# Performance work log

Hardware: AMD Instinct MI355X
Metric: run time of the kernel (lower is better)

The kernel has to match this reference:

```python
import jax, jax.numpy as jnp
import numpy as np

N_AE = 512
N_DE = 256
N = 100000
NUM_SEG = 1024
EPS = 1e-5


def setup_inputs() -> dict:
    key = jax.random.key(0)
    ks = jax.random.split(key, 20)
    d_in1 = 2 * N_AE + N_DE  # 1280
    inp = {
        "x": jax.random.normal(ks[0], (N, 2 * N_AE), dtype=jnp.float32),
        "dist_feat": jax.random.normal(ks[1], (N, N_DE), dtype=jnp.float32),
        "atom_idx": jax.random.randint(ks[2], (N,), 0, 100, dtype=jnp.int32),
        "ele_idx": jax.random.randint(ks[3], (N,), 0, NUM_SEG, dtype=jnp.int32),
        # layer 1 params
        "l1_w": jax.random.normal(ks[4], (d_in1, N_AE), dtype=jnp.float32) * (1.0 / np.sqrt(d_in1)),
        "l1_b": jnp.zeros((N_AE,), dtype=jnp.float32),
        "l1_g": jnp.ones((N_AE,), dtype=jnp.float32),
        "l1_be": jnp.zeros((N_AE,), dtype=jnp.float32),
        # layer 2 params (same input width: 2*n_ae + n_de)
        "l2_w": jax.random.normal(ks[5], (d_in1, N_AE), dtype=jnp.float32) * (1.0 / np.sqrt(d_in1)),
        "l2_b": jnp.zeros((N_AE,), dtype=jnp.float32),
        "l2_g": jnp.ones((N_AE,), dtype=jnp.float32),
        "l2_be": jnp.zeros((N_AE,), dtype=jnp.float32),
        # final fc + bn
        "f_w": jax.random.normal(ks[6], (2 * N_AE, N_AE), dtype=jnp.float32) * (1.0 / np.sqrt(2 * N_AE)),
        "f_b": jnp.zeros((N_AE,), dtype=jnp.float32),
        "f_g": jnp.ones((N_AE,), dtype=jnp.float32),
        "f_be": jnp.zeros((N_AE,), dtype=jnp.float32),
    }
    return inp


def _bn(h, gamma, beta):
    # BatchNorm1d in training mode: batch stats, biased variance
    m = jnp.mean(h, axis=0)
    v = jnp.mean(jnp.square(h - m), axis=0)
    return gamma * (h - m) * jax.lax.rsqrt(v + EPS) + beta


def _dist_layer(x_cat, ele_idx, w, b, gamma, beta):
    h = jax.nn.relu(_bn(x_cat @ w + b, gamma, beta))  # [N, n_ae]
    sums = jax.ops.segment_sum(h, ele_idx, num_segments=NUM_SEG)  # [S, n_ae]
    cnt = jax.ops.segment_sum(jnp.ones((h.shape[0],), h.dtype), ele_idx, num_segments=NUM_SEG)
    mean = sums / jnp.maximum(cnt, 1.0)[:, None]
    return jnp.concatenate([h, mean[ele_idx]], axis=1)  # [N, 2*n_ae]


def reference(x, dist_feat, atom_idx, ele_idx,
              l1_w, l1_b, l1_g, l1_be,
              l2_w, l2_b, l2_g, l2_be,
              f_w, f_b, f_g, f_be):
    h = _dist_layer(jnp.concatenate([x, dist_feat], axis=1), ele_idx, l1_w, l1_b, l1_g, l1_be)
    h = _dist_layer(jnp.concatenate([h, dist_feat], axis=1), ele_idx, l2_w, l2_b, l2_g, l2_be)
    out = jax.nn.relu(_bn(h @ f_w + f_b, f_g, f_be))  # [N, n_ae]
    return out
```

## Files before the change

### kernel.cpp

```cpp
#include <hip/hip_runtime.h>
#include <stdint.h>
#include <stdio.h>

#define NOUT 512
#define NSEG 1024

typedef unsigned short u16;
typedef __attribute__((ext_vector_type(4))) float f32x4;
typedef __attribute__((ext_vector_type(8))) short s16x8;
typedef __attribute__((ext_vector_type(4))) unsigned short u16x4;

__device__ __forceinline__ u16 f2b(float f) {
  union { float f; uint32_t u; } v; v.f = f;
  uint32_t r = v.u + 0x7FFFu + ((v.u >> 16) & 1u);
  return (u16)(r >> 16);
}
__device__ __forceinline__ float b2f(u16 b) {
  union { uint32_t u; float f; } v; v.u = ((uint32_t)b) << 16;
  return v.f;
}

typedef __attribute__((address_space(1))) const void GAS;
typedef __attribute__((address_space(3))) void LAS;
__device__ __forceinline__ void llds16(const void* g, void* l) {
  __builtin_amdgcn_global_load_lds((GAS*)g, (LAS*)l, 16, 0, 0);
}

__global__ void k_cast(const float* __restrict__ src, u16* __restrict__ dst, long n4) {
  long i = blockIdx.x * (long)blockDim.x + threadIdx.x;
  long stride = (long)gridDim.x * blockDim.x;
  for (; i < n4; i += stride) {
    float4 v = reinterpret_cast<const float4*>(src)[i];
    u16x4 o;
    o.x = f2b(v.x); o.y = f2b(v.y); o.z = f2b(v.z); o.w = f2b(v.w);
    reinterpret_cast<u16x4*>(dst)[i] = o;
  }
}

__global__ void k_wtcastT(const float* __restrict__ w, u16* __restrict__ out, int K) {
  __shared__ float tile[32][33];
  int k0 = blockIdx.x * 32, c0 = blockIdx.y * 32;
  int t = threadIdx.x;
  int rr = t >> 5, cc = t & 31;
#pragma unroll
  for (int p = 0; p < 4; ++p)
    tile[p * 8 + rr][cc] = w[(long)(k0 + p * 8 + rr) * NOUT + c0 + cc];
  __syncthreads();
#pragma unroll
  for (int p = 0; p < 4; ++p)
    out[(long)(c0 + p * 8 + rr) * K + k0 + cc] = f2b(tile[cc][p * 8 + rr]);
}

__global__ void k_hist(const int* __restrict__ ele, int* __restrict__ cnt, int N) {
  int i = blockIdx.x * blockDim.x + threadIdx.x;
  int stride = gridDim.x * blockDim.x;
  for (; i < N; i += stride) atomicAdd(&cnt[ele[i]], 1);
}

__global__ void k_scan(const int* __restrict__ cnt, int* __restrict__ off) {
  __shared__ int tmp[NSEG];
  int t = threadIdx.x;
  tmp[t] = cnt[t];
  __syncthreads();
  for (int o = 1; o < NSEG; o <<= 1) {
    int add = (t >= o) ? tmp[t - o] : 0;
    __syncthreads();
    tmp[t] += add;
    __syncthreads();
  }
  off[t] = tmp[t] - cnt[t];
}

__global__ void k_scatter(const int* __restrict__ ele, const int* __restrict__ off,
                          int* __restrict__ fill, int* __restrict__ rows, int N) {
  int i = blockIdx.x * blockDim.x + threadIdx.x;
  int stride = gridDim.x * blockDim.x;
  for (; i < N; i += stride) {
    int e = ele[i];
    int p = atomicAdd(&fill[e], 1);
    rows[off[e] + p] = i;
  }
}

__global__ void k_finalize(const float* __restrict__ sum, const float* __restrict__ sumsq,
                           const float* __restrict__ g, const float* __restrict__ be,
                           float* __restrict__ A, float* __restrict__ C, int M) {
  int c = threadIdx.x;
  float m = sum[c] / (float)M;
  float v = sumsq[c] / (float)M - m * m;
  float a = g[c] * rsqrtf(v + 1e-5f);
  A[c] = a;
  C[c] = be[c] - a * m;
}

__global__ void k_bnseg(const u16* __restrict__ hp, u16* __restrict__ h, u16* __restrict__ mean,
                        const float* __restrict__ A, const float* __restrict__ C,
                        const int* __restrict__ off, const int* __restrict__ cnt,
                        const int* __restrict__ rows) {
  int s = blockIdx.x;
  int c0 = 2 * threadIdx.x;
  int n = cnt[s], o = off[s];
  float a0 = A[c0], a1 = A[c0 + 1], cc0 = C[c0], cc1 = C[c0 + 1];
  float s0 = 0.f, s1 = 0.f;
#pragma unroll 2
  for (int j = 0; j < n; ++j) {
    int r = rows[o + j];
    uint32_t v = *reinterpret_cast<const uint32_t*>(&hp[(long)r * NOUT + c0]);
    float h0 = fmaxf(a0 * b2f((u16)(v & 0xffff)) + cc0, 0.f);
    float h1 = fmaxf(a1 * b2f((u16)(v >> 16)) + cc1, 0.f);
    s0 += h0; s1 += h1;
    *reinterpret_cast<uint32_t*>(&h[(long)r * NOUT + c0]) =
        ((uint32_t)f2b(h1) << 16) | (uint32_t)f2b(h0);
  }
  float inv = 1.f / fmaxf((float)n, 1.f);
  *reinterpret_cast<uint32_t*>(&mean[(long)s * NOUT + c0]) =
      ((uint32_t)f2b(s1 * inv) << 16) | (uint32_t)f2b(s0 * inv);
}

__global__ void k_final(const u16* __restrict__ hp, float* __restrict__ out,
                        const float* __restrict__ A, const float* __restrict__ C, long n4) {
  long i = blockIdx.x * (long)blockDim.x + threadIdx.x;
  long stride = (long)gridDim.x * blockDim.x;
  for (; i < n4; i += stride) {
    u16x4 v = reinterpret_cast<const u16x4*>(hp)[i];
    int c0 = (int)((i * 4) & (NOUT - 1));
    float4 a = *reinterpret_cast<const float4*>(&A[c0]);
    float4 c = *reinterpret_cast<const float4*>(&C[c0]);
    float4 o;
    o.x = fmaxf(a.x * b2f(v.x) + c.x, 0.f);
    o.y = fmaxf(a.y * b2f(v.y) + c.y, 0.f);
    o.z = fmaxf(a.z * b2f(v.z) + c.z, 0.f);
    o.w = fmaxf(a.w * b2f(v.w) + c.w, 0.f);
    reinterpret_cast<float4*>(out)[i] = o;
  }
}

__global__ __launch_bounds__(256, 4) void k_gemm(
    const u16* p0, const u16* p1, int e0, int w0, int w1, int g0, int g1,
    const int* __restrict__ ele,
    const u16* __restrict__ wbt, int ldb, int e0b, int bskip,
    const float* __restrict__ tab, int addtab,
    u16* __restrict__ outp, float* __restrict__ outf, int wf32,
    float* __restrict__ csum, float* __restrict__ csq, int dostats,
    int M, int K) {
  __shared__ __align__(16) u16 As[2 * 4096];
  __shared__ __align__(16) u16 Bs[2 * 4096];

  int nwg = gridDim.x;
  int orig = blockIdx.x;
  int q = nwg >> 3, r8 = nwg & 7;
  int xcd = orig & 7, loc = orig >> 3;
  int bid = (xcd < r8 ? xcd * (q + 1) : r8 * (q + 1) + (xcd - r8) * q) + loc;
  int mt = bid >> 2, ct = bid & 3;
  int brow = mt * 128, bcol = ct * 128;

  int tid = (int)threadIdx.x;
  int lane = tid & 63;
  int wid = tid >> 6;
  int wr = wid >> 1, wc = wid & 1;
  int l15 = lane & 15, kg = lane >> 4;

  int srow = tid >> 2;
  int soct = ((tid & 3) ^ ((srow >> 1) & 3)) * 8;

  int gr0 = brow + srow, gr1 = gr0 + 64;
  int gr0c = gr0 < M ? gr0 : M - 1;
  int gr1c = gr1 < M ? gr1 : M - 1;
  int el0 = ele[gr0c], el1 = ele[gr1c];

  const u16* a00 = p0 + (long)(g0 ? el0 : gr0c) * w0 + soct;
  const u16* a01 = p1 + (long)(g1 ? el0 : gr0c) * w1 + soct - e0;
  const u16* a10 = p0 + (long)(g0 ? el1 : gr1c) * w0 + soct;
  const u16* a11 = p1 + (long)(g1 ? el1 : gr1c) * w1 + soct - e0;

  const u16* b0p = wbt + (long)(bcol + srow) * ldb + soct;
  const u16* b1p = wbt + (long)(bcol + srow + 64) * ldb + soct;

  int xoct = (kg ^ ((l15 >> 1) & 3)) * 8;
  int aro = (wr * 64 + l15) * 32 + xoct;
  int bro = (wc * 64 + l15) * 32 + xoct;

  f32x4 acc[4][4];
#pragma unroll
  for (int m = 0; m < 4; ++m)
#pragma unroll
    for (int n = 0; n < 4; ++n)
#pragma unroll
      for (int j = 0; j < 4; ++j) acc[m][n][j] = 0.f;

  int KT = K >> 5;
  int dst = wid * 512;

  auto stage = [&](int tt, int buf) {
    int k0 = tt << 5;
    const u16* sa0 = k0 < e0 ? a00 : a01;
    const u16* sa1 = k0 < e0 ? a10 : a11;
    int bo = k0 + (k0 >= e0b ? bskip : 0);
    int ab = buf * 4096 + dst;
    llds16(sa0 + k0, &As[ab]);
    llds16(sa1 + k0, &As[ab + 2048]);
    llds16(b0p + bo, &Bs[ab]);
    llds16(b1p + bo, &Bs[ab + 2048]);
  };

  stage(0, 0);
  __syncthreads();

  for (int t = 0; t < KT; ++t) {
    int cur = t & 1;
    if (t + 1 < KT) stage(t + 1, cur ^ 1);
    __builtin_amdgcn_sched_barrier(0);
    const u16* Ab = &As[cur * 4096];
    const u16* Bb = &Bs[cur * 4096];
    s16x8 af[4], bf[4];
#pragma unroll
    for (int m = 0; m < 4; ++m)
      af[m] = *reinterpret_cast<const s16x8*>(&Ab[m * 512 + aro]);
#pragma unroll
    for (int n = 0; n < 4; ++n)
      bf[n] = *reinterpret_cast<const s16x8*>(&Bb[n * 512 + bro]);
#pragma unroll
    for (int m = 0; m < 4; ++m)
#pragma unroll
      for (int n = 0; n < 4; ++n)
        acc[m][n] = __builtin_amdgcn_mfma_f32_16x16x32_bf16(af[m], bf[n], acc[m][n], 0, 0, 0);
    __syncthreads();
  }

  float sums[4] = {0.f, 0.f, 0.f, 0.f}, sqs[4] = {0.f, 0.f, 0.f, 0.f};
#pragma unroll
  for (int m = 0; m < 4; ++m) {
    int row0 = brow + wr * 64 + m * 16 + kg * 4;
#pragma unroll
    for (int j = 0; j < 4; ++j) {
      int r = row0 + j;
      if (r < M) {
        long rb = (long)r * NOUT;
        long tb = addtab ? (long)ele[r] * NOUT : 0;
#pragma unroll
        for (int n = 0; n < 4; ++n) {
          int col = bcol + wc * 64 + n * 16 + l15;
          float v = acc[m][n][j];
          if (addtab) v += tab[tb + col];
          if (wf32) outf[rb + col] = v;
          else outp[rb + col] = f2b(v);
          sums[n] += v;
          sqs[n] += v * v;
        }
      }
    }
  }
  if (dostats) {
#pragma unroll
    for (int n = 0; n < 4; ++n) {
      sums[n] += __shfl_xor(sums[n], 16);
      sums[n] += __shfl_xor(sums[n], 32);
      sqs[n] += __shfl_xor(sqs[n], 16);
      sqs[n] += __shfl_xor(sqs[n], 32);
    }
    if (kg == 0) {
#pragma unroll
      for (int n = 0; n < 4; ++n) {
        int col = bcol + wc * 64 + n * 16 + l15;
        atomicAdd(&csum[col], sums[n]);
        atomicAdd(&csq[col], sqs[n]);
      }
    }
  }
}

extern "C" void kernel_launch(void* const* d_in, const int* in_sizes, int n_in,
                              void* d_out, int out_size, void* d_ws, size_t ws_size,
                              hipStream_t stream) {
  const float* x    = (const float*)d_in[0];
  const float* dist = (const float*)d_in[1];
  const int* ele    = (const int*)d_in[3];
  const float* l1w  = (const float*)d_in[4];
  const float* l1g  = (const float*)d_in[6];
  const float* l1be = (const float*)d_in[7];
  const float* l2w  = (const float*)d_in[8];
  const float* l2g  = (const float*)d_in[10];
  const float* l2be = (const float*)d_in[11];
  const float* fw   = (const float*)d_in[12];
  const float* fg   = (const float*)d_in[14];
  const float* fbe  = (const float*)d_in[15];

  int N = in_sizes[0] / 1024;
  float* out = (float*)d_out;
  u16* xbf = (u16*)d_out;

  int MT = (N + 127) / 128;

  char* w = (char*)d_ws;
  auto alloc = [&](size_t bytes) {
    char* p = w;
    w += (bytes + 255) & ~(size_t)255;
    return p;
  };
  u16* dist_bf = (u16*)alloc((size_t)N * 256 * 2);
  u16* hp      = (u16*)alloc((size_t)N * NOUT * 2);
  u16* h       = (u16*)alloc((size_t)N * NOUT * 2);
  u16* mean    = (u16*)alloc((size_t)NSEG * NOUT * 2);
  u16* w1bt    = (u16*)alloc((size_t)NOUT * 1280 * 2);
  u16* w2bt    = (u16*)alloc((size_t)NOUT * 1280 * 2);
  u16* fbt     = (u16*)alloc((size_t)NOUT * 1024 * 2);
  float* mc2   = (float*)alloc((size_t)NSEG * NOUT * 4);
  float* mc3   = (float*)alloc((size_t)NSEG * NOUT * 4);
  float* colsum = (float*)alloc(NOUT * 4 * 2);
  float* colsumsq = colsum + NOUT;
  float* bnA   = (float*)alloc(NOUT * 4);
  float* bnC   = (float*)alloc(NOUT * 4);
  int* seg_cnt = (int*)alloc(NSEG * 4);
  int* seg_off = (int*)alloc(NSEG * 4);
  int* seg_fill = (int*)alloc(NSEG * 4);
  int* rows    = (int*)alloc((size_t)N * 4);

  size_t need = (size_t)(w - (char*)d_ws);
  if (need > ws_size) {
    fprintf(stderr, "kernel_launch: ws too small: need %zu have %zu\n", need, ws_size);
    return;
  }

  long n4x = (long)N * 1024 / 4;
  long n4d = (long)N * 256 / 4;
  long n4h = (long)N * NOUT / 4;
  int gemmGrid = MT * 4;
  int mcGrid = (NSEG / 128) * 4;

  k_cast<<<4096, 256, 0, stream>>>(x, xbf, n4x);
  k_cast<<<2048, 256, 0, stream>>>(dist, dist_bf, n4d);
  dim3 wt1(1280 / 32, 16), wt3(1024 / 32, 16);
  k_wtcastT<<<wt1, 256, 0, stream>>>(l1w, w1bt, 1280);
  k_wtcastT<<<wt1, 256, 0, stream>>>(l2w, w2bt, 1280);
  k_wtcastT<<<wt3, 256, 0, stream>>>(fw, fbt, 1024);

  hipMemsetAsync(seg_cnt, 0, NSEG * 4, stream);
  hipMemsetAsync(seg_fill, 0, NSEG * 4, stream);
  k_hist<<<512, 256, 0, stream>>>(ele, seg_cnt, N);
  k_scan<<<1, NSEG, 0, stream>>>(seg_cnt, seg_off);
  k_scatter<<<512, 256, 0, stream>>>(ele, seg_off, seg_fill, rows, N);

  hipMemsetAsync(colsum, 0, NOUT * 4 * 2, stream);
  k_gemm<<<gemmGrid, 256, 0, stream>>>(xbf, dist_bf, 1024, 1024, 256, 0, 0, ele,
                                       w1bt, 1280, 1280, 0, mc2, 0,
                                       hp, mc2, 0, colsum, colsumsq, 1, N, 1280);
  k_finalize<<<1, NOUT, 0, stream>>>(colsum, colsumsq, l1g, l1be, bnA, bnC, N);
  k_bnseg<<<NSEG, 256, 0, stream>>>(hp, h, mean, bnA, bnC, seg_off, seg_cnt, rows);

  k_gemm<<<mcGrid, 256, 0, stream>>>(mean, mean, 512, 512, 512, 0, 0, ele,
                                     w2bt + 512, 1280, 512, 0, mc2, 0,
                                     hp, mc2, 1, colsum, colsumsq, 0, NSEG, 512);
  hipMemsetAsync(colsum, 0, NOUT * 4 * 2, stream);
  k_gemm<<<gemmGrid, 256, 0, stream>>>(h, dist_bf, 512, 512, 256, 0, 0, ele,
                                       w2bt, 1280, 512, 512, mc2, 1,
                                       hp, mc2, 0, colsum, colsumsq, 1, N, 768);
  k_finalize<<<1, NOUT, 0, stream>>>(colsum, colsumsq, l2g, l2be, bnA, bnC, N);
  k_bnseg<<<NSEG, 256, 0, stream>>>(hp, h, mean, bnA, bnC, seg_off, seg_cnt, rows);

  k_gemm<<<mcGrid, 256, 0, stream>>>(mean, mean, 512, 512, 512, 0, 0, ele,
                                     fbt + 512, 1024, 512, 0, mc3, 0,
                                     hp, mc3, 1, colsum, colsumsq, 0, NSEG, 512);
  hipMemsetAsync(colsum, 0, NOUT * 4 * 2, stream);
  k_gemm<<<gemmGrid, 256, 0, stream>>>(h, h, 512, 512, 512, 0, 0, ele,
                                       fbt, 1024, 512, 0, mc3, 1,
                                       hp, mc3, 0, colsum, colsumsq, 1, N, 512);
  k_finalize<<<1, NOUT, 0, stream>>>(colsum, colsumsq, fg, fbe, bnA, bnC, N);
  k_final<<<4096, 256, 0, stream>>>(hp, out, bnA, bnC, n4h);
}
```

Measured before the change: 951.2 us.

## Fuse fp32-to-bf16 input casts into GEMM A-tile loading and vectorize epilogue

Removes the separate cast kernels for x and dist_feat and their bf16 copies. The GEMM now loads fp32 A tiles straight into registers, converts them to bf16 after the MFMA step and writes them to LDS, overlapping the load with compute. This saves one full read-and-write pass over the large inputs, at the cost of more registers and VALU work inside the GEMM. The MFMA operands are also swapped so each lane holds four consecutive columns, which lets the epilogue use vectorized stores and table reads, with a wider shuffle reduction for the column statistics.

```diff
diff --git a/kernel.cpp b/kernel.cpp
--- a/kernel.cpp
+++ b/kernel.cpp
@@ -24,17 +24,6 @@
 typedef __attribute__((address_space(3))) void LAS;
 __device__ __forceinline__ void llds16(const void* g, void* l) {
   __builtin_amdgcn_global_load_lds((GAS*)g, (LAS*)l, 16, 0, 0);
-}
-
-__global__ void k_cast(const float* __restrict__ src, u16* __restrict__ dst, long n4) {
-  long i = blockIdx.x * (long)blockDim.x + threadIdx.x;
-  long stride = (long)gridDim.x * blockDim.x;
-  for (; i < n4; i += stride) {
-    float4 v = reinterpret_cast<const float4*>(src)[i];
-    u16x4 o;
-    o.x = f2b(v.x); o.y = f2b(v.y); o.z = f2b(v.z); o.w = f2b(v.w);
-    reinterpret_cast<u16x4*>(dst)[i] = o;
-  }
 }
 
 __global__ void k_wtcastT(const float* __restrict__ w, u16* __restrict__ out, int K) {
@@ -135,8 +124,10 @@
   }
 }
 
+template <bool FA0, bool FA1>
 __global__ __launch_bounds__(256, 4) void k_gemm(
-    const u16* p0, const u16* p1, int e0, int w0, int w1, int g0, int g1,
+    const u16* p0, const u16* p1, const float* f0, const float* f1,
+    int e0, int w0, int w1, int g0, int g1,
     const int* __restrict__ ele,
     const u16* __restrict__ wbt, int ldb, int e0b, int bskip,
     const float* __restrict__ tab, int addtab,
@@ -163,18 +154,36 @@
   int srow = tid >> 2;
   int soct = ((tid & 3) ^ ((srow >> 1) & 3)) * 8;
 
-  int gr0 = brow + srow, gr1 = gr0 + 64;
-  int gr0c = gr0 < M ? gr0 : M - 1;
-  int gr1c = gr1 < M ? gr1 : M - 1;
-  int el0 = ele[gr0c], el1 = ele[gr1c];
-
-  const u16* a00 = p0 + (long)(g0 ? el0 : gr0c) * w0 + soct;
-  const u16* a01 = p1 + (long)(g1 ? el0 : gr0c) * w1 + soct - e0;
-  const u16* a10 = p0 + (long)(g0 ? el1 : gr1c) * w0 + soct;
-  const u16* a11 = p1 + (long)(g1 ? el1 : gr1c) * w1 + soct - e0;
-
+  const u16 *a00 = nullptr, *a01 = nullptr, *a10 = nullptr, *a11 = nullptr;
+  if constexpr (!FA0 || !FA1) {
+    int gr0 = brow + srow, gr1 = gr0 + 64;
+    int gr0c = gr0 < M ? gr0 : M - 1;
+    int gr1c = gr1 < M ? gr1 : M - 1;
+    int el0 = (g0 | g1) ? ele[gr0c] : 0, el1 = (g0 | g1) ? ele[gr1c] : 0;
+    a00 = p0 + (long)(g0 ? el0 : gr0c) * w0 + soct;
+    a01 = p1 + (long)(g1 ? el0 : gr0c) * w1 + soct;
+    a10 = p0 + (long)(g0 ? el1 : gr1c) * w0 + soct;
+    a11 = p1 + (long)(g1 ? el1 : gr1c) * w1 + soct;
+  }
   const u16* b0p = wbt + (long)(bcol + srow) * ldb + soct;
   const u16* b1p = wbt + (long)(bcol + srow + 64) * ldb + soct;
+
+  int fs = tid & 7;
+  int fr = tid >> 3;
+  long fro0[4], fro1[4];
+  int fdst[4];
+  if constexpr (FA0 || FA1) {
+#pragma unroll
+    for (int i = 0; i < 4; ++i) {
+      int rl = fr + 32 * i;
+      int gr = brow + rl;
+      if (gr >= M) gr = M - 1;
+      fro0[i] = (long)gr * w0;
+      fro1[i] = (long)gr * w1;
+      fdst[i] = rl * 32 + (fs ^ ((((rl >> 1) & 3)) << 1)) * 4;
+    }
+  }
+  float4 la[4];
 
   int xoct = (kg ^ ((l15 >> 1) & 3)) * 8;
   int aro = (wr * 64 + l15) * 32 + xoct;
@@ -191,24 +200,64 @@
   int KT = K >> 5;
   int dst = wid * 512;
 
-  auto stage = [&](int tt, int buf) {
+  auto issueA = [&](int tt, int buf) {
     int k0 = tt << 5;
-    const u16* sa0 = k0 < e0 ? a00 : a01;
-    const u16* sa1 = k0 < e0 ? a10 : a11;
+    if (k0 < e0) {
+      if constexpr (FA0) {
+#pragma unroll
+        for (int i = 0; i < 4; ++i)
+          la[i] = *reinterpret_cast<const float4*>(f0 + fro0[i] + k0 + fs * 4);
+      } else {
+        int ab = buf * 4096 + dst;
+        llds16(a00 + k0, &As[ab]);
+        llds16(a10 + k0, &As[ab + 2048]);
+      }
+    } else {
+      int ko = k0 - e0;
+      if constexpr (FA1) {
+#pragma unroll
+        for (int i = 0; i < 4; ++i)
+          la[i] = *reinterpret_cast<const float4*>(f1 + fro1[i] + ko + fs * 4);
+      } else {
+        int ab = buf * 4096 + dst;
+        llds16(a01 + ko, &As[ab]);
+        llds16(a11 + ko, &As[ab + 2048]);
+      }
+    }
+  };
+  auto commitA = [&](int tt, int buf) {
+    int k0 = tt << 5;
+    bool isf = (k0 < e0) ? FA0 : FA1;
+    if (isf) {
+      int ab = buf * 4096;
+#pragma unroll
+      for (int i = 0; i < 4; ++i) {
+        u16x4 pk;
+        pk.x = f2b(la[i].x); pk.y = f2b(la[i].y);
+        pk.z = f2b(la[i].z); pk.w = f2b(la[i].w);
+        *reinterpret_cast<u16x4*>(&As[ab + fdst[i]]) = pk;
+      }
+    }
+  };
+  auto issueB = [&](int tt, int buf) {
+    int k0 = tt << 5;
     int bo = k0 + (k0 >= e0b ? bskip : 0);
     int ab = buf * 4096 + dst;
-    llds16(sa0 + k0, &As[ab]);
-    llds16(sa1 + k0, &As[ab + 2048]);
     llds16(b0p + bo, &Bs[ab]);
     llds16(b1p + bo, &Bs[ab + 2048]);
   };
 
-  stage(0, 0);
+  issueA(0, 0);
+  issueB(0, 0);
+  commitA(0, 0);
   __syncthreads();
 
   for (int t = 0; t < KT; ++t) {
     int cur = t & 1;
-    if (t + 1 < KT) stage(t + 1, cur ^ 1);
+    if (t + 1 < KT) {
+      issueA(t + 1, cur ^ 1);
+      issueB(t + 1, cur ^ 1);
+    }
     __builtin_amdgcn_sched_barrier(0);
     const u16* Ab = &As[cur * 4096];
     const u16* Bb = &Bs[cur * 4096];
@@ -223,47 +272,63 @@
     for (int m = 0; m < 4; ++m)
 #pragma unroll
       for (int n = 0; n < 4; ++n)
-        acc[m][n] = __builtin_amdgcn_mfma_f32_16x16x32_bf16(af[m], bf[n], acc[m][n], 0, 0, 0);
+        acc[m][n] = __builtin_amdgcn_mfma_f32_16x16x32_bf16(bf[n], af[m], acc[m][n], 0, 0, 0);
+    __builtin_amdgcn_sched_barrier(0);
+    if (t + 1 < KT) commitA(t + 1, cur ^ 1);
     __syncthreads();
   }
 
-  float sums[4] = {0.f, 0.f, 0.f, 0.f}, sqs[4] = {0.f, 0.f, 0.f, 0.f};
+  f32x4 sums4[4], sqs4[4];
+#pragma unroll
+  for (int n = 0; n < 4; ++n)
+#pragma unroll
+    for (int j = 0; j < 4; ++j) { sums4[n][j] = 0.f; sqs4[n][j] = 0.f; }
 #pragma unroll
   for (int m = 0; m < 4; ++m) {
-    int row0 = brow + wr * 64 + m * 16 + kg * 4;
-#pragma unroll
-    for (int j = 0; j < 4; ++j) {
-      int r = row0 + j;
-      if (r < M) {
-        long rb = (long)r * NOUT;
-        long tb = addtab ? (long)ele[r] * NOUT : 0;
-#pragma unroll
-        for (int n = 0; n < 4; ++n) {
-          int col = bcol + wc * 64 + n * 16 + l15;
-          float v = acc[m][n][j];
-          if (addtab) v += tab[tb + col];
-          if (wf32) outf[rb + col] = v;
-          else outp[rb + col] = f2b(v);
-          sums[n] += v;
-          sqs[n] += v * v;
+    int row = brow + wr * 64 + m * 16 + l15;
+    bool ok = row < M;
+    long rb = (long)(ok ? row : 0) * NOUT;
+    long tb = (addtab && ok) ? (long)ele[row] * NOUT : 0;
+#pragma unroll
+    for (int n = 0; n < 4; ++n) {
+      int col0 = bcol + wc * 64 + n * 16 + kg * 4;
+      f32x4 v = acc[m][n];
+      if (addtab && ok) {
+        float4 tv = *reinterpret_cast<const float4*>(&tab[tb + col0]);
+        v[0] += tv.x; v[1] += tv.y; v[2] += tv.z; v[3] += tv.w;
+      }
+      if (ok) {
+        if (wf32) {
+          *reinterpret_cast<f32x4*>(&outf[rb + col0]) = v;
+        } else {
+          u16x4 pk;
+          pk.x = f2b(v[0]); pk.y = f2b(v[1]); pk.z = f2b(v[2]); pk.w = f2b(v[3]);
+          *reinterpret_cast<u16x4*>(&outp[rb + col0]) = pk;
         }
+#pragma unroll
+        for (int j = 0; j < 4; ++j) { sums4[n][j] += v[j]; sqs4[n][j] += v[j] * v[j]; }
       }
     }
   }
   if (dostats) {
 #pragma unroll
-    for (int n = 0; n < 4; ++n) {
-      sums[n] += __shfl_xor(sums[n], 16);
-      sums[n] += __shfl_xor(sums[n], 32);
-      sqs[n] += __shfl_xor(sqs[n], 16);
-      sqs[n] += __shfl_xor(sqs[n], 32);
-    }
-    if (kg == 0) {
+    for (int n = 0; n < 4; ++n)
+#pragma unroll
+      for (int d = 1; d < 16; d <<= 1)
+#pragma unroll
+        for (int j = 0; j < 4; ++j) {
+          sums4[n][j] += __shfl_xor(sums4[n][j], d);
+          sqs4[n][j] += __shfl_xor(sqs4[n][j], d);
+        }
+    if (l15 == 0) {
 #pragma unroll
       for (int n = 0; n < 4; ++n) {
-        int col = bcol + wc * 64 + n * 16 + l15;
-        atomicAdd(&csum[col], sums[n]);
-        atomicAdd(&csq[col], sqs[n]);
+        int col0 = bcol + wc * 64 + n * 16 + kg * 4;
+#pragma unroll
+        for (int j = 0; j < 4; ++j) {
+          atomicAdd(&csum[col0 + j], sums4[n][j]);
+          atomicAdd(&csq[col0 + j], sqs4[n][j]);
+        }
       }
     }
   }
@@ -287,7 +352,6 @@
 
   int N = in_sizes[0] / 1024;
   float* out = (float*)d_out;
-  u16* xbf = (u16*)d_out;
 
   int MT = (N + 127) / 128;
 
@@ -297,7 +361,6 @@
     w += (bytes + 255) & ~(size_t)255;
     return p;
   };
-  u16* dist_bf = (u16*)alloc((size_t)N * 256 * 2);
   u16* hp      = (u16*)alloc((size_t)N * NOUT * 2);
   u16* h       = (u16*)alloc((size_t)N * NOUT * 2);
   u16* mean    = (u16*)alloc((size_t)NSEG * NOUT * 2);
@@ -321,14 +384,10 @@
     return;
   }
 
-  long n4x = (long)N * 1024 / 4;
-  long n4d = (long)N * 256 / 4;
   long n4h = (long)N * NOUT / 4;
   int gemmGrid = MT * 4;
   int mcGrid = (NSEG / 128) * 4;
 
-  k_cast<<<4096, 256, 0, stream>>>(x, xbf, n4x);
-  k_cast<<<2048, 256, 0, stream>>>(dist, dist_bf, n4d);
   dim3 wt1(1280 / 32, 16), wt3(1024 / 32, 16);
   k_wtcastT<<<wt1, 256, 0, stream>>>(l1w, w1bt, 1280);
   k_wtcastT<<<wt1, 256, 0, stream>>>(l2w, w2bt, 1280);
@@ -341,29 +400,34 @@
   k_scatter<<<512, 256, 0, stream>>>(ele, seg_off, seg_fill, rows, N);
 
   hipMemsetAsync(colsum, 0, NOUT * 4 * 2, stream);
-  k_gemm<<<gemmGrid, 256, 0, stream>>>(xbf, dist_bf, 1024, 1024, 256, 0, 0, ele,
-                                       w1bt, 1280, 1280, 0, mc2, 0,
-                                       hp, mc2, 0, colsum, colsumsq, 1, N, 1280);
+  k_gemm<true, true><<<gemmGrid, 256, 0, stream>>>(
+      hp, hp, x, dist, 1024, 1024, 256, 0, 0, ele,
+      w1bt, 1280, 1280, 0, mc2, 0,
+      hp, mc2, 0, colsum, colsumsq, 1, N, 1280);
   k_finalize<<<1, NOUT, 0, stream>>>(colsum, colsumsq, l1g, l1be, bnA, bnC, N);
   k_bnseg<<<NSEG, 256, 0, stream>>>(hp, h, mean, bnA, bnC, seg_off, seg_cnt, rows);
 
-  k_gemm<<<mcGrid, 256, 0, stream>>>(mean, mean, 512, 512, 512, 0, 0, ele,
-                                     w2bt + 512, 1280, 512, 0, mc2, 0,
-                                     hp, mc2, 1, colsum, colsumsq, 0, NSEG, 512);
+  k_gemm<false, false><<<mcGrid, 256, 0, stream>>>(
+      mean, mean, x, dist, 512, 512, 512, 0, 0, ele,
+      w2bt + 512, 1280, 512, 0, mc2, 0,
+      hp, mc2, 1, colsum, colsumsq, 0, NSEG, 512);
   hipMemsetAsync(colsum, 0, NOUT * 4 * 2, stream);
-  k_gemm<<<gemmGrid, 256, 0, stream>>>(h, dist_bf, 512, 512, 256, 0, 0, ele,
-                                       w2bt, 1280, 512, 512, mc2, 1,
-                                       hp, mc2, 0, colsum, colsumsq, 1, N, 768);
+  k_gemm<false, true><<<gemmGrid, 256, 0, stream>>>(
+      h, hp, x, dist, 512, 512, 256, 0, 0, ele,
+      w2bt, 1280, 512, 512, mc2, 1,
+      hp, mc2, 0, colsum, colsumsq, 1, N, 768);
   k_finalize<<<1, NOUT, 0, stream>>>(colsum, colsumsq, l2g, l2be, bnA, bnC, N);
   k_bnseg<<<NSEG, 256, 0, stream>>>(hp, h, mean, bnA, bnC, seg_off, seg_cnt, rows);
 
-  k_gemm<<<mcGrid, 256, 0, stream>>>(mean, mean, 512, 512, 512, 0, 0, ele,
-                                     fbt + 512, 1024, 512, 0, mc3, 0,
-                                     hp, mc3, 1, colsum, colsumsq, 0, NSEG, 512);
+  k_gemm<false, false><<<mcGrid, 256, 0, stream>>>(
+      mean, mean, x, dist, 512, 512, 512, 0, 0, ele,
+      fbt + 512, 1024, 512, 0, mc3, 0,
+      hp, mc3, 1, colsum, colsumsq, 0, NSEG, 512);
   hipMemsetAsync(colsum, 0, NOUT * 4 * 2, stream);
-  k_gemm<<<gemmGrid, 256, 0, stream>>>(h, h, 512, 512, 512, 0, 0, ele,
-                                       fbt, 1024, 512, 0, mc3, 1,
-                                       hp, mc3, 0, colsum, colsumsq, 1, N, 512);
+  k_gemm<false, false><<<gemmGrid, 256, 0, stream>>>(
+      h, h, x, dist, 512, 512, 512, 0, 0, ele,
+      fbt, 1024, 512, 0, mc3, 1,
+      hp, mc3, 0, colsum, colsumsq, 1, N, 512);
   k_finalize<<<1, NOUT, 0, stream>>>(colsum, colsumsq, fg, fbe, bnA, bnC, N);
   k_final<<<4096, 256, 0, stream>>>(hp, out, bnA, bnC, n4h);
 }
```

Result: slower. 3.480 ms (+265.8%).
